# Optimization experiments

Measured on AMD Instinct MI355X. Metric: run time of the kernel, lower is better.

The kernel has to match this reference:

```python
import jax, jax.numpy as jnp
import numpy as np
from jax import lax


def _conv(x, w, b):
    # NCHW x OIHW, stride 1, padding 2 (k=5 'same')
    y = lax.conv_general_dilated(
        x, w, window_strides=(1, 1), padding=((2, 2), (2, 2)),
        dimension_numbers=("NCHW", "OIHW", "NCHW"))
    return y + b[None, :, None, None]


def _maxpool(x, pad):
    return lax.reduce_window(
        x, -jnp.inf, lax.max,
        window_dimensions=(1, 1, 2, 2), window_strides=(1, 1, 2, 2),
        padding=((0, 0), (0, 0), (pad, pad), (pad, pad)))


def setup_inputs() -> dict:
    key = jax.random.key(0)
    ks = jax.random.split(key, 12)
    B = 8192
    x = jax.random.normal(ks[0], (B, 1, 28, 28), dtype=jnp.float32)

    def conv_params(kw, kb, cout, cin, k=5):
        w = jax.random.uniform(kw, (cout, cin, k, k), jnp.float32, -1.0, 1.0)
        bound = 1.0 / np.sqrt(cin * k * k)
        b = jax.random.uniform(kb, (cout,), jnp.float32, -bound, bound)
        return w, b

    def fc_params(kw, kb, cout, cin):
        w = jax.random.uniform(kw, (cout, cin), jnp.float32, -1.0, 1.0)
        bound = 1.0 / np.sqrt(cin)
        b = jax.random.uniform(kb, (cout,), jnp.float32, -bound, bound)
        return w, b

    w1, b1 = conv_params(ks[1], ks[2], 16, 1)
    w2, b2 = conv_params(ks[3], ks[4], 32, 16)
    w3, b3 = conv_params(ks[5], ks[6], 64, 32)
    fw1, fb1 = fc_params(ks[7], ks[8], 256, 1024)
    fw2, fb2 = fc_params(ks[9], ks[10], 10, 256)
    return {"x": x, "w1": w1, "b1": b1, "w2": w2, "b2": b2,
            "w3": w3, "b3": b3, "fw1": fw1, "fb1": fb1,
            "fw2": fw2, "fb2": fb2}


def reference(x, w1, b1, w2, b2, w3, b3, fw1, fb1, fw2, fb2):
    h = jax.nn.relu(_conv(x, w1, b1))          # [B,16,28,28]
    h = _maxpool(h, 0)                          # [B,16,14,14]
    h = jax.nn.relu(_conv(h, w2, b2))           # [B,32,14,14]
    h = _maxpool(h, 0)                          # [B,32,7,7]
    h = jax.nn.relu(_conv(h, w3, b3))           # [B,64,7,7]
    h = _maxpool(h, 1)                          # [B,64,4,4]
    h = h.reshape(h.shape[0], -1)               # [B,1024]
    h = jax.nn.relu(h @ fw1.T + fb1)            # [B,256]
    h = h @ fw2.T + fb2                         # [B,10]
    return jax.nn.log_softmax(h, axis=1)
```

## Files before the change

kernel.cpp:

```cpp
#include <hip/hip_runtime.h>
#include <hip/hip_bf16.h>
#include <math.h>


typedef short bf16x8 __attribute__((ext_vector_type(8)));
typedef float f32x4 __attribute__((ext_vector_type(4)));
typedef unsigned short u16;
#define MFMA16 __builtin_amdgcn_mfma_f32_16x16x32_bf16

__device__ __forceinline__ u16 f2b(float f) {
  __hip_bfloat16 h = __float2bfloat16(f);
  return *reinterpret_cast<u16*>(&h);
}

__global__ __launch_bounds__(256) void mega_pack(
    const float* __restrict__ w2, const float* __restrict__ w3,
    const float* __restrict__ fw1, const float* __restrict__ w1,
    u16* __restrict__ Bp2, u16* __restrict__ Bp3,
    u16* __restrict__ Bp1, u16* __restrict__ Bp0) {
  int gid = blockIdx.x * 256 + threadIdx.x;
  if (gid < 13312) {
    int i = gid;
    int j = i & 7, lane = (i >> 3) & 63, nt = (i >> 9) & 1, c = i >> 10;
    int tap = 2 * c + (lane >> 5);
    int ci = ((lane >> 4) & 1) * 8 + j;
    int co = nt * 16 + (lane & 15);
    float v = (tap < 25) ? w2[co * 400 + ci * 25 + tap] : 0.f;
    Bp2[i] = f2b(v);
  } else if (gid < 64512) {
    int i = gid - 13312;
    int j = i & 7, lane = (i >> 3) & 63, nt = (i >> 9) & 3, c = i >> 11;
    int ci = (lane >> 4) * 8 + j;
    int co = nt * 16 + (lane & 15);
    Bp3[i] = f2b(w3[co * 800 + ci * 25 + c]);
  } else if (gid < 326656) {
    int i = gid - 64512;
    int j = i & 7, lane = (i >> 3) & 63, nt = (i >> 9) & 15, c = i >> 13;
    int k = c * 32 + (lane >> 4) * 8 + j;
    int col = nt * 16 + (lane & 15);
    Bp1[i] = f2b(fw1[col * 1024 + k]);
  } else {
    int i = gid - 326656;
    int j = i & 7, lane = (i >> 3) & 63, pc = i >> 9;
    int px = pc % 28, c = pc / 28;
    int co = lane & 15;
    int xp = (lane >> 4) * 8 + j;
    int kx = xp - px;
    float v = (kx >= 0 && kx < 5) ? w1[co * 25 + c * 5 + kx] : 0.f;
    Bp0[i] = f2b(v);
  }
}

__global__ __launch_bounds__(448) void conv1_mfma(
    const float* __restrict__ x, const u16* __restrict__ Bp0,
    const float* __restrict__ b1, u16* __restrict__ p1) {
  __shared__ u16 img_s[16 * 1280];
  const int imgG = blockIdx.x;
  const int t = threadIdx.x;
  const int w = t >> 6, l = t & 63;
  const int co = l & 15, g = l >> 4;
  const int p0 = w * 4;

  bf16x8 Bfr[5][4];
#pragma unroll
  for (int c = 0; c < 5; ++c)
#pragma unroll
    for (int q = 0; q < 4; ++q)
      Bfr[c][q] = *(const bf16x8*)(Bp0 + ((size_t)(c * 28 + p0 + q) << 9) + l * 8);

  const int4 z4 = make_int4(0, 0, 0, 0);
  for (int i = t; i < 2560; i += 448) ((int4*)img_s)[i] = z4;
  __syncthreads();
  const float2* xg = (const float2*)(x + (size_t)imgG * 16 * 784);
  for (int i = t; i < 6272; i += 448) {
    int p = i / 14, xc = (i % 14) * 2;
    float2 v = xg[i];
    int img = p / 28, y = p % 28;
    unsigned pk = (unsigned)f2b(v.x) | ((unsigned)f2b(v.y) << 16);
    *(unsigned*)(img_s + img * 1280 + (y + 2) * 40 + xc + 2) = pk;
  }
  __syncthreads();

  const float bias = b1[co];
  const int pxp0 = p0 >> 1;
  for (int mt = 0; mt < 28; ++mt) {
    int m = mt * 16 + co;
    int imgA = m / 28, py = m - imgA * 28;
    const u16* ap = img_s + imgA * 1280 + py * 40 + g * 8;
    f32x4 a0 = (f32x4){bias, bias, bias, bias};
    f32x4 a1 = a0, a2 = a0, a3 = a0;
#pragma unroll
    for (int c = 0; c < 5; ++c) {
      bf16x8 av = *(const bf16x8*)(ap + c * 40);
      a0 = MFMA16(av, Bfr[c][0], a0, 0, 0, 0);
      a1 = MFMA16(av, Bfr[c][1], a1, 0, 0, 0);
      a2 = MFMA16(av, Bfr[c][2], a2, 0, 0, 0);
      a3 = MFMA16(av, Bfr[c][3], a3, 0, 0, 0);
    }
    int m0 = mt * 16 + g * 4;
    int imgC = m0 / 28, py0 = m0 - imgC * 28;
    size_t base = ((size_t)((imgG * 16 + imgC) * 196)) << 4;
    int pyp0 = py0 >> 1;
#pragma unroll
    for (int h = 0; h < 2; ++h) {
      float vA = fmaxf(fmaxf(a0[2 * h], a0[2 * h + 1]),
                       fmaxf(a1[2 * h], a1[2 * h + 1]));
      float vB = fmaxf(fmaxf(a2[2 * h], a2[2 * h + 1]),
                       fmaxf(a3[2 * h], a3[2 * h + 1]));
      p1[base + (((size_t)(pyp0 + h) * 14 + pxp0) << 4) + co]     = f2b(fmaxf(vA, 0.f));
      p1[base + (((size_t)(pyp0 + h) * 14 + pxp0 + 1) << 4) + co] = f2b(fmaxf(vB, 0.f));
    }
  }
}

__global__ __launch_bounds__(256) void conv2_mfma(
    const u16* __restrict__ p1, const u16* __restrict__ Bp2,
    const float* __restrict__ b2, u16* __restrict__ p2) {
  __shared__ u16 smem[15552];
  const int bb = blockIdx.x;
  const int t = threadIdx.x;
  const int w = t >> 6, l = t & 63;

  for (int i = t; i < 15552; i += 256) smem[i] = 0;
  __syncthreads();
  for (int i = t; i < 784; i += 256) {
    int half = i & 1, xx = (i >> 1) % 14, y = ((i >> 1) / 14) % 14, img = i / 392;
    const int4 v = *(const int4*)(p1 + (((size_t)(bb * 2 + img) * 196 + y * 14 + xx) << 4) + half * 8);
    *(int4*)(smem + img * 7776 + ((y + 2) * 18 + (xx + 2)) * 24 + half * 8) = v;
  }
  __syncthreads();

  const int g = l >> 4;
  const int cil = (g & 1) * 8;
  const int tapadd = g >> 1;
  const int nmt = (w == 0) ? 7 : 6;

  int abase[7];
#pragma unroll
  for (int jj = 0; jj < 7; ++jj) {
    int mt = w + jj * 4;
    int m = mt * 16 + (l & 15); if (m > 391) m = 391;
    int img = m / 196, pix = m % 196;
    int py = pix / 14, px = pix % 14;
    abase[jj] = img * 7776 + (py * 18 + px) * 24 + cil;
  }
  const float bias0 = b2[l & 15], bias1 = b2[16 + (l & 15)];
  f32x4 acc[7][2];
#pragma unroll
  for (int jj = 0; jj < 7; ++jj) {
    acc[jj][0] = (f32x4){bias0, bias0, bias0, bias0};
    acc[jj][1] = (f32x4){bias1, bias1, bias1, bias1};
  }
  const bf16x8* Bb = (const bf16x8*)Bp2;
  bf16x8 b0 = Bb[l], b1 = Bb[64 + l];
  for (int c = 0; c < 13; ++c) {
    bf16x8 n0 = b0, n1 = b1;
    if (c < 12) { n0 = Bb[((c + 1) * 2) * 64 + l]; n1 = Bb[((c + 1) * 2 + 1) * 64 + l]; }
    int tp = 2 * c + tapadd; if (tp > 24) tp = 24;
    int ky = tp / 5, kx = tp - ky * 5;
    int off = (ky * 18 + kx) * 24;
#pragma unroll
    for (int jj = 0; jj < 7; ++jj) {
      if (jj < nmt) {
        bf16x8 a = *(const bf16x8*)(smem + abase[jj] + off);
        acc[jj][0] = MFMA16(a, b0, acc[jj][0], 0, 0, 0);
        acc[jj][1] = MFMA16(a, b1, acc[jj][1], 0, 0, 0);
      }
    }
    b0 = n0; b1 = n1;
  }
  __syncthreads();
#pragma unroll
  for (int jj = 0; jj < 7; ++jj) {
    if (jj < nmt) {
      int mt = w + jj * 4;
#pragma unroll
      for (int r = 0; r < 4; ++r) {
        int m = mt * 16 + (l >> 4) * 4 + r;
        if (m < 392) {
          int img = m / 196, pix = m % 196;
          smem[img * 6272 + (l & 15) * 196 + pix]        = f2b(fmaxf(acc[jj][0][r], 0.f));
          smem[img * 6272 + (16 + (l & 15)) * 196 + pix] = f2b(fmaxf(acc[jj][1][r], 0.f));
        }
      }
    }
  }
  __syncthreads();
  for (int i = t; i < 3136; i += 256) {
    int co = i & 31, p = (i >> 5) % 49, img = i / 1568;
    int oy = p / 7, ox = p % 7;
    int base = img * 6272 + co * 196 + oy * 28 + ox * 2;
    u16 m0 = smem[base], m1 = smem[base + 1], m2 = smem[base + 14], m3 = smem[base + 15];
    u16 a = m0 > m1 ? m0 : m1, bq = m2 > m3 ? m2 : m3;
    p2[(((size_t)(bb * 2 + img) * 49 + p) << 5) + co] = a > bq ? a : bq;
  }
}

__global__ __launch_bounds__(256) void conv3_mfma(
    const u16* __restrict__ p2, const u16* __restrict__ Bp3,
    const float* __restrict__ b3, u16* __restrict__ p3) {
  __shared__ u16 smem[19360];
  const int bb = blockIdx.x;
  const int t = threadIdx.x;
  const int w = t >> 6, l = t & 63;

  for (int i = t; i < 19360; i += 256) smem[i] = 0;
  __syncthreads();
  for (int i = t; i < 784; i += 256) {
    int oct = i & 3, xx = (i >> 2) % 7, y = ((i >> 2) / 7) % 7, img = i / 196;
    const int4 v = *(const int4*)(p2 + (((size_t)(bb * 4 + img) * 49 + y * 7 + xx) << 5) + oct * 8);
    *(int4*)(smem + img * 4840 + ((y + 2) * 11 + (xx + 2)) * 40 + oct * 8) = v;
  }
  __syncthreads();

  const int g = l >> 4;
  const int cil = g * 8;
  const int nmt = (w == 0) ? 4 : 3;

  int abase[4];
#pragma unroll
  for (int jj = 0; jj < 4; ++jj) {
    int mt = w + jj * 4;
    int m = mt * 16 + (l & 15); if (m > 195) m = 195;
    int img = m / 49, pix = m % 49;
    int py = pix / 7, px = pix % 7;
    abase[jj] = img * 4840 + (py * 11 + px) * 40 + cil;
  }
  f32x4 acc[4][4];
#pragma unroll
  for (int q = 0; q < 4; ++q) {
    float bias = b3[q * 16 + (l & 15)];
#pragma unroll
    for (int jj = 0; jj < 4; ++jj)
      acc[jj][q] = (f32x4){bias, bias, bias, bias};
  }
  const bf16x8* Bb = (const bf16x8*)Bp3;
  bf16x8 bfr[4];
#pragma unroll
  for (int q = 0; q < 4; ++q) bfr[q] = Bb[q * 64 + l];
  for (int c = 0; c < 25; ++c) {
    bf16x8 nb0 = bfr[0], nb1 = bfr[1], nb2 = bfr[2], nb3 = bfr[3];
    if (c < 24) {
      nb0 = Bb[((c + 1) * 4 + 0) * 64 + l];
      nb1 = Bb[((c + 1) * 4 + 1) * 64 + l];
      nb2 = Bb[((c + 1) * 4 + 2) * 64 + l];
      nb3 = Bb[((c + 1) * 4 + 3) * 64 + l];
    }
    int ky = c / 5, kx = c - ky * 5;
    int off = (ky * 11 + kx) * 40;
#pragma unroll
    for (int jj = 0; jj < 4; ++jj) {
      if (jj < nmt) {
        bf16x8 a = *(const bf16x8*)(smem + abase[jj] + off);
        acc[jj][0] = MFMA16(a, bfr[0], acc[jj][0], 0, 0, 0);
        acc[jj][1] = MFMA16(a, bfr[1], acc[jj][1], 0, 0, 0);
        acc[jj][2] = MFMA16(a, bfr[2], acc[jj][2], 0, 0, 0);
        acc[jj][3] = MFMA16(a, bfr[3], acc[jj][3], 0, 0, 0);
      }
    }
    bfr[0] = nb0; bfr[1] = nb1; bfr[2] = nb2; bfr[3] = nb3;
  }
  __syncthreads();
#pragma unroll
  for (int jj = 0; jj < 4; ++jj) {
    if (jj < nmt) {
      int mt = w + jj * 4;
#pragma unroll
      for (int q = 0; q < 4; ++q)
#pragma unroll
        for (int r = 0; r < 4; ++r) {
          int m = mt * 16 + (l >> 4) * 4 + r;
          if (m < 196) {
            int img = m / 49, pix = m % 49;
            smem[img * 3136 + (q * 16 + (l & 15)) * 49 + pix] = f2b(fmaxf(acc[jj][q][r], 0.f));
          }
        }
    }
  }
  __syncthreads();
  for (int i = t; i < 4096; i += 256) {
    int co = i & 63, p = (i >> 6) % 16, img = i >> 10;
    int oy = p >> 2, ox = p & 3;
    int y0 = oy ? 2 * oy - 1 : 0, y1 = 2 * oy;
    int x0 = ox ? 2 * ox - 1 : 0, x1 = 2 * ox;
    u16 mm = 0;
    for (int y = y0; y <= y1; ++y)
      for (int xx = x0; xx <= x1; ++xx) {
        u16 v = smem[img * 3136 + co * 49 + y * 7 + xx];
        if (v > mm) mm = v;
      }
    p3[(((size_t)(bb * 4 + img)) << 10) + co * 16 + p] = mm;
  }
}

__global__ __launch_bounds__(256) void fc1_mfma(
    const u16* __restrict__ p3, const u16* __restrict__ Bp1,
    const float* __restrict__ fb1, float* __restrict__ h4) {
  const int bid = blockIdx.x;
  const int mb = bid >> 1, nb = bid & 1;
  const int t = threadIdx.x;
  const int w = t >> 6, l = t & 63;
  const int g = l >> 4;

  const int mt0 = mb * 4 + (w >> 1) * 2;
  const int ntbase = nb * 8 + (w & 1) * 4;

  size_t arow0 = (size_t)(mt0 * 16 + (l & 15)) * 1024 + g * 8;
  size_t arow1 = arow0 + 16 * 1024;
  const bf16x8* Bb = (const bf16x8*)Bp1;

  f32x4 acc[2][4];
#pragma unroll
  for (int i = 0; i < 2; ++i)
#pragma unroll
    for (int q = 0; q < 4; ++q) acc[i][q] = (f32x4){0.f, 0.f, 0.f, 0.f};

  bf16x8 a0 = *(const bf16x8*)(p3 + arow0);
  bf16x8 a1 = *(const bf16x8*)(p3 + arow1);
  bf16x8 bq0 = Bb[(ntbase + 0) * 64 + l], bq1 = Bb[(ntbase + 1) * 64 + l];
  bf16x8 bq2 = Bb[(ntbase + 2) * 64 + l], bq3 = Bb[(ntbase + 3) * 64 + l];

  for (int c = 0; c < 32; ++c) {
    bf16x8 na0 = a0, na1 = a1, nb0 = bq0, nb1 = bq1, nb2 = bq2, nb3 = bq3;
    if (c < 31) {
      na0 = *(const bf16x8*)(p3 + arow0 + (c + 1) * 32);
      na1 = *(const bf16x8*)(p3 + arow1 + (c + 1) * 32);
      nb0 = Bb[((c + 1) * 16 + ntbase + 0) * 64 + l];
      nb1 = Bb[((c + 1) * 16 + ntbase + 1) * 64 + l];
      nb2 = Bb[((c + 1) * 16 + ntbase + 2) * 64 + l];
      nb3 = Bb[((c + 1) * 16 + ntbase + 3) * 64 + l];
    }
    acc[0][0] = MFMA16(a0, bq0, acc[0][0], 0, 0, 0);
    acc[0][1] = MFMA16(a0, bq1, acc[0][1], 0, 0, 0);
    acc[0][2] = MFMA16(a0, bq2, acc[0][2], 0, 0, 0);
    acc[0][3] = MFMA16(a0, bq3, acc[0][3], 0, 0, 0);
    acc[1][0] = MFMA16(a1, bq0, acc[1][0], 0, 0, 0);
    acc[1][1] = MFMA16(a1, bq1, acc[1][1], 0, 0, 0);
    acc[1][2] = MFMA16(a1, bq2, acc[1][2], 0, 0, 0);
    acc[1][3] = MFMA16(a1, bq3, acc[1][3], 0, 0, 0);
    a0 = na0; a1 = na1; bq0 = nb0; bq1 = nb1; bq2 = nb2; bq3 = nb3;
  }
#pragma unroll
  for (int i = 0; i < 2; ++i) {
    int mrow = (mt0 + i) * 16 + g * 4;
#pragma unroll
    for (int q = 0; q < 4; ++q) {
      int col = (ntbase + q) * 16 + (l & 15);
      float bias = fb1[col];
#pragma unroll
      for (int r = 0; r < 4; ++r)
        h4[(size_t)(mrow + r) * 256 + col] = fmaxf(acc[i][q][r] + bias, 0.f);
    }
  }
}

__global__ __launch_bounds__(256) void fc2_lsm(
    const float* __restrict__ h4, const float* __restrict__ fw2,
    const float* __restrict__ fb2, float* __restrict__ out) {
  const int wave = threadIdx.x >> 6;
  const int lane = threadIdx.x & 63;
  const int b = blockIdx.x * 4 + wave;
  const float* h = h4 + (size_t)b * 256;
  float acc[10];
#pragma unroll
  for (int o = 0; o < 10; ++o) acc[o] = 0.f;
#pragma unroll
  for (int j = 0; j < 4; ++j) {
    const float a = h[lane + j * 64];
#pragma unroll
    for (int o = 0; o < 10; ++o)
      acc[o] = fmaf(a, fw2[o * 256 + lane + j * 64], acc[o]);
  }
#pragma unroll
  for (int o = 0; o < 10; ++o)
    for (int s = 32; s > 0; s >>= 1) acc[o] += __shfl_down(acc[o], s, 64);
  if (lane == 0) {
    float v[10], m = -1e30f;
#pragma unroll
    for (int o = 0; o < 10; ++o) { v[o] = acc[o] + fb2[o]; m = fmaxf(m, v[o]); }
    float s = 0.f;
#pragma unroll
    for (int o = 0; o < 10; ++o) s += expf(v[o] - m);
    const float lse = m + logf(s);
#pragma unroll
    for (int o = 0; o < 10; ++o) out[(size_t)b * 10 + o] = v[o] - lse;
  }
}

extern "C" void kernel_launch(void* const* d_in, const int* in_sizes, int n_in,
                              void* d_out, int out_size, void* d_ws, size_t ws_size,
                              hipStream_t stream) {
  const float* x   = (const float*)d_in[0];
  const float* w1  = (const float*)d_in[1];
  const float* b1  = (const float*)d_in[2];
  const float* w2  = (const float*)d_in[3];
  const float* b2  = (const float*)d_in[4];
  const float* w3  = (const float*)d_in[5];
  const float* b3  = (const float*)d_in[6];
  const float* fw1 = (const float*)d_in[7];
  const float* fb1 = (const float*)d_in[8];
  const float* fw2 = (const float*)d_in[9];
  const float* fb2 = (const float*)d_in[10];
  float* out = (float*)d_out;

  char* W = (char*)d_ws;
  u16*   p1  = (u16*)(W);
  u16*   p2  = (u16*)(W + 51380224);
  u16*   p3  = (u16*)(W + 77070336);
  float* h4  = (float*)(W + 93847552);
  u16*   Bp2 = (u16*)(W + 102236160);
  u16*   Bp3 = (u16*)(W + 102262784);
  u16*   Bp1 = (u16*)(W + 102365184);
  u16*   Bp0 = (u16*)(W + 102889472);

  mega_pack <<<dim3(1556), dim3(256), 0, stream>>>(w2, w3, fw1, w1, Bp2, Bp3, Bp1, Bp0);
  conv1_mfma<<<dim3(512),  dim3(448), 0, stream>>>(x, Bp0, b1, p1);
  conv2_mfma<<<dim3(4096), dim3(256), 0, stream>>>(p1, Bp2, b2, p2);
  conv3_mfma<<<dim3(2048), dim3(256), 0, stream>>>(p2, Bp3, b3, p3);
  fc1_mfma<<<dim3(256), dim3(256), 0, stream>>>(p3, Bp1, fb1, h4);
  fc2_lsm<<<dim3(2048), dim3(256), 0, stream>>>(h4, fw2, fb2, out);
}
```

Baseline: 277.2 us.

## Fuse maxpool into conv2/conv3 MFMA epilogues via pool-window row ordering

Reorders the GEMM M dimension in conv2 and conv3 so that each lane's four accumulator rows are the four pixels of one 2x2 pooling window. Pooling then happens in registers and results go straight to global memory, which removes the shared-memory staging, two barriers and the separate pooling pass. Conv3 pads its rows to 64 per image (4x4 windows with border clamping), so all waves run 4 tiles and some MFMA work is redundant. Shared-memory zeroing is also vectorized to int4 stores.

Result: faster. 241.7 us (-12.8%).

```diff
diff --git a/kernel.cpp b/kernel.cpp
--- a/kernel.cpp
+++ b/kernel.cpp
@@ -121,7 +121,8 @@
   const int t = threadIdx.x;
   const int w = t >> 6, l = t & 63;
 
-  for (int i = t; i < 15552; i += 256) smem[i] = 0;
+  const int4 z4 = make_int4(0, 0, 0, 0);
+  for (int i = t; i < 1944; i += 256) ((int4*)smem)[i] = z4;
   __syncthreads();
   for (int i = t; i < 784; i += 256) {
     int half = i & 1, xx = (i >> 1) % 14, y = ((i >> 1) / 14) % 14, img = i / 392;
@@ -133,18 +134,20 @@
   const int g = l >> 4;
   const int cil = (g & 1) * 8;
   const int tapadd = g >> 1;
+  const int col = l & 15;
   const int nmt = (w == 0) ? 7 : 6;
 
   int abase[7];
 #pragma unroll
   for (int jj = 0; jj < 7; ++jj) {
-    int mt = w + jj * 4;
-    int m = mt * 16 + (l & 15); if (m > 391) m = 391;
-    int img = m / 196, pix = m % 196;
-    int py = pix / 14, px = pix % 14;
+    int m = (w + jj * 4) * 16 + col; if (m > 391) m = 391;
+    int img = m / 196, rel = m - img * 196;
+    int wl = rel >> 2, e = rel & 3;
+    int oy = wl / 7, ox = wl - oy * 7;
+    int py = 2 * oy + (e >> 1), px = 2 * ox + (e & 1);
     abase[jj] = img * 7776 + (py * 18 + px) * 24 + cil;
   }
-  const float bias0 = b2[l & 15], bias1 = b2[16 + (l & 15)];
+  const float bias0 = b2[col], bias1 = b2[16 + col];
   f32x4 acc[7][2];
 #pragma unroll
   for (int jj = 0; jj < 7; ++jj) {
@@ -169,30 +172,22 @@
     }
     b0 = n0; b1 = n1;
   }
-  __syncthreads();
 #pragma unroll
   for (int jj = 0; jj < 7; ++jj) {
     if (jj < nmt) {
-      int mt = w + jj * 4;
-#pragma unroll
-      for (int r = 0; r < 4; ++r) {
-        int m = mt * 16 + (l >> 4) * 4 + r;
-        if (m < 392) {
-          int img = m / 196, pix = m % 196;
-          smem[img * 6272 + (l & 15) * 196 + pix]        = f2b(fmaxf(acc[jj][0][r], 0.f));
-          smem[img * 6272 + (16 + (l & 15)) * 196 + pix] = f2b(fmaxf(acc[jj][1][r], 0.f));
-        }
+      int m0 = (w + jj * 4) * 16 + g * 4;
+      if (m0 < 392) {
+        int img = m0 / 196, rel = m0 - img * 196;
+        int wl = rel >> 2;
+        float v0 = fmaxf(fmaxf(acc[jj][0][0], acc[jj][0][1]),
+                         fmaxf(acc[jj][0][2], acc[jj][0][3]));
+        float v1 = fmaxf(fmaxf(acc[jj][1][0], acc[jj][1][1]),
+                         fmaxf(acc[jj][1][2], acc[jj][1][3]));
+        size_t base = (((size_t)(bb * 2 + img) * 49 + wl) << 5);
+        p2[base + col]      = f2b(fmaxf(v0, 0.f));
+        p2[base + 16 + col] = f2b(fmaxf(v1, 0.f));
       }
     }
-  }
-  __syncthreads();
-  for (int i = t; i < 3136; i += 256) {
-    int co = i & 31, p = (i >> 5) % 49, img = i / 1568;
-    int oy = p / 7, ox = p % 7;
-    int base = img * 6272 + co * 196 + oy * 28 + ox * 2;
-    u16 m0 = smem[base], m1 = smem[base + 1], m2 = smem[base + 14], m3 = smem[base + 15];
-    u16 a = m0 > m1 ? m0 : m1, bq = m2 > m3 ? m2 : m3;
-    p2[(((size_t)(bb * 2 + img) * 49 + p) << 5) + co] = a > bq ? a : bq;
   }
 }
 
@@ -204,7 +199,8 @@
   const int t = threadIdx.x;
   const int w = t >> 6, l = t & 63;
 
-  for (int i = t; i < 19360; i += 256) smem[i] = 0;
+  const int4 z4 = make_int4(0, 0, 0, 0);
+  for (int i = t; i < 2420; i += 256) ((int4*)smem)[i] = z4;
   __syncthreads();
   for (int i = t; i < 784; i += 256) {
     int oct = i & 3, xx = (i >> 2) % 7, y = ((i >> 2) / 7) % 7, img = i / 196;
@@ -215,21 +211,23 @@
 
   const int g = l >> 4;
   const int cil = g * 8;
-  const int nmt = (w == 0) ? 4 : 3;
+  const int col = l & 15;
 
   int abase[4];
 #pragma unroll
   for (int jj = 0; jj < 4; ++jj) {
-    int mt = w + jj * 4;
-    int m = mt * 16 + (l & 15); if (m > 195) m = 195;
-    int img = m / 49, pix = m % 49;
-    int py = pix / 7, px = pix % 7;
+    int m = (w + jj * 4) * 16 + col;
+    int img = m >> 6, rel = m & 63;
+    int wa = rel >> 2, e = rel & 3;
+    int oy = wa >> 2, ox = wa & 3;
+    int py = 2 * oy + (e >> 1) - 1; if (py < 0) py = 0;
+    int px = 2 * ox + (e & 1) - 1;  if (px < 0) px = 0;
     abase[jj] = img * 4840 + (py * 11 + px) * 40 + cil;
   }
   f32x4 acc[4][4];
 #pragma unroll
   for (int q = 0; q < 4; ++q) {
-    float bias = b3[q * 16 + (l & 15)];
+    float bias = b3[q * 16 + col];
 #pragma unroll
     for (int jj = 0; jj < 4; ++jj)
       acc[jj][q] = (f32x4){bias, bias, bias, bias};
@@ -250,46 +248,29 @@
     int off = (ky * 11 + kx) * 40;
 #pragma unroll
     for (int jj = 0; jj < 4; ++jj) {
-      if (jj < nmt) {
-        bf16x8 a = *(const bf16x8*)(smem + abase[jj] + off);
-        acc[jj][0] = MFMA16(a, bfr[0], acc[jj][0], 0, 0, 0);
-        acc[jj][1] = MFMA16(a, bfr[1], acc[jj][1], 0, 0, 0);
-        acc[jj][2] = MFMA16(a, bfr[2], acc[jj][2], 0, 0, 0);
-        acc[jj][3] = MFMA16(a, bfr[3], acc[jj][3], 0, 0, 0);
-      }
+      bf16x8 a = *(const bf16x8*)(smem + abase[jj] + off);
+      acc[jj][0] = MFMA16(a, bfr[0], acc[jj][0], 0, 0, 0);
+      acc[jj][1] = MFMA16(a, bfr[1], acc[jj][1], 0, 0, 0);
+      acc[jj][2] = MFMA16(a, bfr[2], acc[jj][2], 0, 0, 0);
+      acc[jj][3] = MFMA16(a, bfr[3], acc[jj][3], 0, 0, 0);
     }
     bfr[0] = nb0; bfr[1] = nb1; bfr[2] = nb2; bfr[3] = nb3;
   }
-  __syncthreads();
 #pragma unroll
   for (int jj = 0; jj < 4; ++jj) {
-    if (jj < nmt) {
-      int mt = w + jj * 4;
-#pragma unroll
-      for (int q = 0; q < 4; ++q)
-#pragma unroll
-        for (int r = 0; r < 4; ++r) {
-          int m = mt * 16 + (l >> 4) * 4 + r;
-          if (m < 196) {
-            int img = m / 49, pix = m % 49;
-            smem[img * 3136 + (q * 16 + (l & 15)) * 49 + pix] = f2b(fmaxf(acc[jj][q][r], 0.f));
-          }
-        }
-    }
-  }
-  __syncthreads();
-  for (int i = t; i < 4096; i += 256) {
-    int co = i & 63, p = (i >> 6) % 16, img = i >> 10;
-    int oy = p >> 2, ox = p & 3;
-    int y0 = oy ? 2 * oy - 1 : 0, y1 = 2 * oy;
-    int x0 = ox ? 2 * ox - 1 : 0, x1 = 2 * ox;
-    u16 mm = 0;
-    for (int y = y0; y <= y1; ++y)
-      for (int xx = x0; xx <= x1; ++xx) {
-        u16 v = smem[img * 3136 + co * 49 + y * 7 + xx];
-        if (v > mm) mm = v;
-      }
-    p3[(((size_t)(bb * 4 + img)) << 10) + co * 16 + p] = mm;
+    int m0 = (w + jj * 4) * 16 + g * 4;
+    int img = m0 >> 6, rel = m0 & 63;
+    int wa = rel >> 2;
+    int oy = wa >> 2, ox = wa & 3;
+    size_t base = (((size_t)(bb * 4 + img)) << 10) + wa;
+#pragma unroll
+    for (int q = 0; q < 4; ++q) {
+      float v = acc[jj][q][3];
+      if (ox > 0) v = fmaxf(v, acc[jj][q][2]);
+      if (oy > 0) v = fmaxf(v, acc[jj][q][1]);
+      if (oy > 0 && ox > 0) v = fmaxf(v, acc[jj][q][0]);
+      p3[base + (size_t)(q * 16 + col) * 16] = f2b(fmaxf(v, 0.f));
+    }
   }
 }
 
```
